# Kernel tuning notes

Hardware: AMD Instinct MI355X
Metric: run time of the kernel (lower is better)

The kernel has to match this reference:

```python
import jax, jax.numpy as jnp
import numpy as np

NEG_INF = -1e9  # matches masked_fill value in torch code
LRELU_ALPHA = 0.2


def setup_inputs() -> dict:
    key = jax.random.key(0)
    k1, k2, k3, k4 = jax.random.split(key, 4)
    B, N, F_IN, H, DK = 4, 2048, 128, 4, 32
    x = jax.random.normal(k1, (B, N, F_IN), dtype=jnp.float32)
    adj = jax.random.randint(k2, (B, N, N), 0, 2, dtype=jnp.int32)
    # xavier-ish scaled params
    W = jax.random.normal(k3, (H, F_IN, DK), dtype=jnp.float32) * (1.0 / np.sqrt(F_IN))
    a = jax.random.normal(k4, (H, 2 * DK, 1), dtype=jnp.float32) * (1.0 / np.sqrt(2 * DK))
    return {"x": x, "adj": adj, "W": W, "a": a}


def reference(x, adj, W, a):
    B, N, _ = x.shape
    H, _, DK = W.shape
    # h: (B, H, N, DK)
    h = jnp.einsum('bni,hio->bhno', x, W)
    # Split attention vector: e[b,h,i,j] = h_i.a_l + h_j.a_r  (avoids O(N^2 * 2d) concat)
    a_l = a[:, :DK, 0]   # (H, DK)
    a_r = a[:, DK:, 0]   # (H, DK)
    el = jnp.einsum('bhnd,hd->bhn', h, a_l)  # (B, H, N)
    er = jnp.einsum('bhnd,hd->bhn', h, a_r)  # (B, H, N)
    e = el[:, :, :, None] + er[:, :, None, :]          # (B, H, N, N)
    e = jax.nn.leaky_relu(e, negative_slope=LRELU_ALPHA)
    e = jnp.where(adj[:, None, :, :] == 0, NEG_INF, e)
    alpha = jax.nn.softmax(e, axis=-1)                 # dropout is identity (eval)
    h_prime = jnp.einsum('bhij,bhjd->bhid', alpha, h)  # (B, H, N, DK)
    # torch code does h_prime.view(B, N, -1) on contiguous (B,H,N,DK): raw reshape
    out = h_prime.reshape(B, N, H * DK)
    return out
```

## Files before the change

kernel.cpp:

```cpp
#include <hip/hip_runtime.h>
#include <stdint.h>

#define LOG2E 1.4426950408889634f

typedef __bf16 v8bf __attribute__((ext_vector_type(8)));
typedef float v16f __attribute__((ext_vector_type(16)));

static constexpr int B = 4, N = 2048, FIN = 128, H = 4, DK = 32;
static constexpr int IT = N / 32;

__device__ __forceinline__ float exp2_fast(float x) {
#if __has_builtin(__builtin_amdgcn_exp2f)
  return __builtin_amdgcn_exp2f(x);
#else
  float r;
  asm("v_exp_f32 %0, %1" : "=v"(r) : "v"(x));
  return r;
#endif
}

__device__ __forceinline__ unsigned int bf16_rne(float f) {
  unsigned int u = __builtin_bit_cast(unsigned int, f);
  u += 0x7FFFu + ((u >> 16) & 1u);
  return u >> 16;
}

__global__ __launch_bounds__(256) void k_prep(const float* __restrict__ x,
                                              const float* __restrict__ W,
                                              unsigned short* __restrict__ xb,
                                              unsigned short* __restrict__ wtb) {
  int idx = blockIdx.x * 256 + threadIdx.x;
  constexpr int TX = B * N * FIN;
  if (idx < TX) {
    xb[idx] = (unsigned short)bf16_rne(x[idx]);
  } else {
    int j = idx - TX;
    int h = j >> 12, r = j & 4095, d = r >> 7, f = r & 127;
    wtb[j] = (unsigned short)bf16_rne(W[(h * FIN + f) * DK + d]);
  }
}

__global__ __launch_bounds__(256) void k_hproj(const unsigned short* __restrict__ xb,
                                               const unsigned short* __restrict__ wtb,
                                               const float* __restrict__ a,
                                               unsigned short* __restrict__ h_t,
                                               float* __restrict__ el,
                                               float* __restrict__ er) {
  int blk = blockIdx.x;
  int b = blk >> 6, it = blk & 63;
  int tid = threadIdx.x;
  int head = tid >> 6, lane = tid & 63;
  int lrow = lane & 31, kh = lane >> 5;
  int bh = b * H + head;
  int n = it * 32 + lrow;
  const unsigned short* xp = xb + (b * N + n) * FIN + kh * 8;
  const unsigned short* wp = wtb + (head * DK + lrow) * FIN + kh * 8;
  v16f acc = {};
#pragma unroll
  for (int s = 0; s < FIN / 16; ++s) {
    v8bf av = __builtin_bit_cast(v8bf, *(const int4*)(wp + s * 16));
    v8bf bv = __builtin_bit_cast(v8bf, *(const int4*)(xp + s * 16));
    acc = __builtin_amdgcn_mfma_f32_32x32x16_bf16(av, bv, acc, 0, 0, 0);
  }
  float pel = 0.f, per = 0.f;
#pragma unroll
  for (int r = 0; r < 16; ++r) {
    int d = (r & 3) + 8 * (r >> 2) + 4 * kh;
    float hv = acc[r];
    h_t[(bh * DK + d) * N + n] = (unsigned short)bf16_rne(hv);
    pel = fmaf(hv, a[head * 2 * DK + d], pel);
    per = fmaf(hv, a[head * 2 * DK + DK + d], per);
  }
  pel += __shfl_xor(pel, 32);
  per += __shfl_xor(per, 32);
  if (kh == 0) {
    el[bh * N + n] = pel * LOG2E;
    er[bh * N + n] = per * LOG2E;
  }
}

__global__ __launch_bounds__(1024, 8) void k_attn(const int* __restrict__ adj,
                                                  const unsigned short* __restrict__ h_t,
                                                  const float* __restrict__ el,
                                                  const float* __restrict__ er,
                                                  float* __restrict__ pnum,
                                                  float* __restrict__ pden) {
  __shared__ float part4[4][H][1024];
  __shared__ float lsh4[4][H][32];
  int blk = blockIdx.x;
  int bit = blk >> 1, jh = blk & 1;
  int b = bit >> 6, it = bit & 63;
  int tid = threadIdx.x;
  int wave = tid >> 6;
  int head = wave & 3, jq = wave >> 2;
  int lane = tid & 63, lrow = lane & 31, kh = lane >> 5;
  int ig = it * 32 + lrow, bh = b * H + head;

  float eli = el[bh * N + ig];
  int j0 = jh * 1024 + jq * 256 + kh * 8;
  const float* erp = er + bh * N + j0;
  const unsigned short* hp = h_t + (size_t)(bh * DK + lrow) * N + j0;
  const int* ap = adj + ((size_t)(b * N + ig)) * N + j0;

  v16f acc = {};
  float lsum = 0.f;
  int4 A0 = *(const int4*)ap;
  int4 A1 = *(const int4*)(ap + 4);
#pragma unroll
  for (int s = 0; s < 16; ++s) {
    int o = s * 16;
    int4 a0 = A0, a1 = A1;
    if (s + 1 < 16) {
      A0 = *(const int4*)(ap + o + 16);
      A1 = *(const int4*)(ap + o + 20);
    }
    float4 ea = *(const float4*)(erp + o);
    float4 eb = *(const float4*)(erp + o + 4);
    int4 hb = *(const int4*)(hp + o);
    float ev[8] = {ea.x, ea.y, ea.z, ea.w, eb.x, eb.y, eb.z, eb.w};
    int aw[8] = {a0.x, a0.y, a0.z, a0.w, a1.x, a1.y, a1.z, a1.w};
    unsigned ub[8];
#pragma unroll
    for (int k = 0; k < 8; ++k) {
      float tt = eli + ev[k];
      tt = fmaxf(tt, 0.2f * tt);
      float pv = exp2_fast(tt);
      unsigned u = __builtin_bit_cast(unsigned, pv) & 0xFFFF0000u;
      u = aw[k] ? u : 0u;
      ub[k] = u;
      lsum += __builtin_bit_cast(float, u);
    }
    unsigned u0 = __builtin_amdgcn_perm(ub[1], ub[0], 0x07060302u);
    unsigned u1 = __builtin_amdgcn_perm(ub[3], ub[2], 0x07060302u);
    unsigned u2 = __builtin_amdgcn_perm(ub[5], ub[4], 0x07060302u);
    unsigned u3 = __builtin_amdgcn_perm(ub[7], ub[6], 0x07060302u);
    uint4 au = {u0, u1, u2, u3};
    v8bf av = __builtin_bit_cast(v8bf, au);
    v8bf hv = __builtin_bit_cast(v8bf, hb);
    acc = __builtin_amdgcn_mfma_f32_32x32x16_bf16(av, hv, acc, 0, 0, 0);
  }

  lsum += __shfl_xor(lsum, 32);
  if (lane < 32) lsh4[jq][head][lane] = lsum;
#pragma unroll
  for (int r = 0; r < 16; ++r) {
    int rowl = (r & 3) + 8 * (r >> 2) + 4 * kh;
    part4[jq][head][rowl * 32 + lrow] = acc[r];
  }
  __syncthreads();

  int e = tid * 4;
  int rh = e >> 10, rr = e & 1023;
  float4 q0 = *(const float4*)&part4[0][rh][rr];
  float4 q1 = *(const float4*)&part4[1][rh][rr];
  float4 q2 = *(const float4*)&part4[2][rh][rr];
  float4 q3 = *(const float4*)&part4[3][rh][rr];
  float4 s4;
  s4.x = (q0.x + q1.x) + (q2.x + q3.x);
  s4.y = (q0.y + q1.y) + (q2.y + q3.y);
  s4.z = (q0.z + q1.z) + (q2.z + q3.z);
  s4.w = (q0.w + q1.w) + (q2.w + q3.w);
  *(float4*)&pnum[(size_t)blk * 4096 + e] = s4;
  if (tid < 128) {
    float d = (lsh4[0][tid >> 5][tid & 31] + lsh4[1][tid >> 5][tid & 31]) +
              (lsh4[2][tid >> 5][tid & 31] + lsh4[3][tid >> 5][tid & 31]);
    pden[blk * 128 + tid] = d;
  }
}

__global__ __launch_bounds__(1024) void k_final(const float* __restrict__ pnum,
                                                const float* __restrict__ pden,
                                                float* __restrict__ out) {
  int bit = blockIdx.x;
  int b = bit >> 6, it = bit & 63;
  int tid = threadIdx.x;
  int e = tid * 4;
  int rh = e >> 10, ri = (e >> 5) & 31, rd = e & 31;
  size_t p0 = (size_t)(bit * 2) * 4096 + e;
  float4 n0 = *(const float4*)&pnum[p0];
  float4 n1 = *(const float4*)&pnum[p0 + 4096];
  float d = pden[bit * 2 * 128 + rh * 32 + ri] + pden[(bit * 2 + 1) * 128 + rh * 32 + ri];
  float inv = 1.0f / d;
  float4 o;
  o.x = (n0.x + n1.x) * inv;
  o.y = (n0.y + n1.y) * inv;
  o.z = (n0.z + n1.z) * inv;
  o.w = (n0.w + n1.w) * inv;
  *(float4*)&out[(size_t)((b * H + rh) * N + it * 32 + ri) * DK + rd] = o;
}

extern "C" void kernel_launch(void* const* d_in, const int* in_sizes, int n_in,
                              void* d_out, int out_size, void* d_ws, size_t ws_size,
                              hipStream_t stream) {
  const float* x = (const float*)d_in[0];
  const int* adj = (const int*)d_in[1];
  const float* W = (const float*)d_in[2];
  const float* a = (const float*)d_in[3];
  float* out = (float*)d_out;
  char* ws = (char*)d_ws;

  unsigned short* h_t = (unsigned short*)(ws);
  float* el = (float*)(ws + 0x200000);
  float* er = (float*)(ws + 0x220000);
  unsigned short* wtb = (unsigned short*)(ws + 0x240000);
  unsigned short* xb = (unsigned short*)(ws + 0x250000);
  float* pnum = (float*)(ws + 0x450000);
  float* pden = (float*)(ws + 0xC50000);

  hipLaunchKernelGGL(k_prep, dim3((B * N * FIN + H * DK * FIN) / 256), dim3(256), 0, stream,
                     x, W, xb, wtb);
  hipLaunchKernelGGL(k_hproj, dim3(B * IT), dim3(256), 0, stream, xb, wtb, a, h_t, el, er);
  hipLaunchKernelGGL(k_attn, dim3(B * IT * 2), dim3(1024), 0, stream, adj, h_t, el, er, pnum, pden);
  hipLaunchKernelGGL(k_final, dim3(B * IT), dim3(1024), 0, stream, pnum, pden, out);
}
```

Before: 158.2 us.

## Pack adjacency into bitmask in prep kernel and read bits in attention

The prep kernel now also compresses the int32 adjacency matrix into a 1-bit-per-entry mask using wave ballots. The attention kernel reads 8 mask words per lane instead of streaming the full int32 rows, and tests bits to zero masked probabilities. Previously each of the four head waves re-read the same adjacency rows, so the goal is to cut that redundant global traffic. The adjacency prefetch in the loop is replaced by prefetching er and h_t. It adds one full pass over adjacency in the prep kernel plus a small workspace buffer.

Result: faster. 135.9 us (-14.1%).

```diff
diff --git a/kernel.cpp b/kernel.cpp
--- a/kernel.cpp
+++ b/kernel.cpp
@@ -8,6 +8,8 @@
 
 static constexpr int B = 4, N = 2048, FIN = 128, H = 4, DK = 32;
 static constexpr int IT = N / 32;
+static constexpr int PACK_BLOCKS = B * N * N / 1024;
+static constexpr int PREP_BLOCKS = (B * N * FIN + H * DK * FIN) / 256;
 
 __device__ __forceinline__ float exp2_fast(float x) {
 #if __has_builtin(__builtin_amdgcn_exp2f)
@@ -25,11 +27,32 @@
   return u >> 16;
 }
 
-__global__ __launch_bounds__(256) void k_prep(const float* __restrict__ x,
+__global__ __launch_bounds__(256) void k_prep(const int* __restrict__ adj,
+                                              const float* __restrict__ x,
                                               const float* __restrict__ W,
+                                              unsigned int* __restrict__ adjb,
                                               unsigned short* __restrict__ xb,
                                               unsigned short* __restrict__ wtb) {
-  int idx = blockIdx.x * 256 + threadIdx.x;
+  int bid = blockIdx.x;
+  int tid = threadIdx.x;
+  if (bid < PACK_BLOCKS) {
+    int wid = (bid * 256 + tid) >> 6;
+    int lane = tid & 63;
+    const int* p = adj + (size_t)wid * 256 + lane;
+    unsigned long long m0 = __ballot(p[0] != 0);
+    unsigned long long m1 = __ballot(p[64] != 0);
+    unsigned long long m2 = __ballot(p[128] != 0);
+    unsigned long long m3 = __ballot(p[192] != 0);
+    if (lane == 0) {
+      uint4 v0 = {(unsigned)m0, (unsigned)(m0 >> 32), (unsigned)m1, (unsigned)(m1 >> 32)};
+      uint4 v1 = {(unsigned)m2, (unsigned)(m2 >> 32), (unsigned)m3, (unsigned)(m3 >> 32)};
+      uint4* dst = (uint4*)(adjb + (size_t)wid * 8);
+      dst[0] = v0;
+      dst[1] = v1;
+    }
+    return;
+  }
+  int idx = (bid - PACK_BLOCKS) * 256 + tid;
   constexpr int TX = B * N * FIN;
   if (idx < TX) {
     xb[idx] = (unsigned short)bf16_rne(x[idx]);
@@ -79,7 +102,7 @@
   }
 }
 
-__global__ __launch_bounds__(1024, 8) void k_attn(const int* __restrict__ adj,
+__global__ __launch_bounds__(1024, 8) void k_attn(const unsigned int* __restrict__ adjb,
                                                   const unsigned short* __restrict__ h_t,
                                                   const float* __restrict__ el,
                                                   const float* __restrict__ er,
@@ -100,25 +123,29 @@
   int j0 = jh * 1024 + jq * 256 + kh * 8;
   const float* erp = er + bh * N + j0;
   const unsigned short* hp = h_t + (size_t)(bh * DK + lrow) * N + j0;
-  const int* ap = adj + ((size_t)(b * N + ig)) * N + j0;
+
+  const uint4* abp = (const uint4*)(adjb + (size_t)(b * N + ig) * 64 + jh * 32 + jq * 8);
+  uint4 ab0 = abp[0], ab1 = abp[1];
+  unsigned adw[8] = {ab0.x, ab0.y, ab0.z, ab0.w, ab1.x, ab1.y, ab1.z, ab1.w};
+  int shkh = kh * 8;
 
   v16f acc = {};
   float lsum = 0.f;
-  int4 A0 = *(const int4*)ap;
-  int4 A1 = *(const int4*)(ap + 4);
+  float4 Ea = *(const float4*)erp;
+  float4 Eb = *(const float4*)(erp + 4);
+  int4 Hb = *(const int4*)hp;
 #pragma unroll
   for (int s = 0; s < 16; ++s) {
-    int o = s * 16;
-    int4 a0 = A0, a1 = A1;
+    float4 ea = Ea, eb = Eb;
+    int4 hb = Hb;
     if (s + 1 < 16) {
-      A0 = *(const int4*)(ap + o + 16);
-      A1 = *(const int4*)(ap + o + 20);
+      int o = (s + 1) * 16;
+      Ea = *(const float4*)(erp + o);
+      Eb = *(const float4*)(erp + o + 4);
+      Hb = *(const int4*)(hp + o);
     }
-    float4 ea = *(const float4*)(erp + o);
-    float4 eb = *(const float4*)(erp + o + 4);
-    int4 hb = *(const int4*)(hp + o);
+    unsigned mb = (adw[s >> 1] >> (((s & 1) * 16) + shkh)) & 0xFFu;
     float ev[8] = {ea.x, ea.y, ea.z, ea.w, eb.x, eb.y, eb.z, eb.w};
-    int aw[8] = {a0.x, a0.y, a0.z, a0.w, a1.x, a1.y, a1.z, a1.w};
     unsigned ub[8];
 #pragma unroll
     for (int k = 0; k < 8; ++k) {
@@ -126,7 +153,7 @@
       tt = fmaxf(tt, 0.2f * tt);
       float pv = exp2_fast(tt);
       unsigned u = __builtin_bit_cast(unsigned, pv) & 0xFFFF0000u;
-      u = aw[k] ? u : 0u;
+      u = (mb & (1u << k)) ? u : 0u;
       ub[k] = u;
       lsum += __builtin_bit_cast(float, u);
     }
@@ -203,13 +230,14 @@
   float* el = (float*)(ws + 0x200000);
   float* er = (float*)(ws + 0x220000);
   unsigned short* wtb = (unsigned short*)(ws + 0x240000);
-  unsigned short* xb = (unsigned short*)(ws + 0x250000);
-  float* pnum = (float*)(ws + 0x450000);
-  float* pden = (float*)(ws + 0xC50000);
-
-  hipLaunchKernelGGL(k_prep, dim3((B * N * FIN + H * DK * FIN) / 256), dim3(256), 0, stream,
-                     x, W, xb, wtb);
+  unsigned int* adjb = (unsigned int*)(ws + 0x250000);
+  unsigned short* xb = (unsigned short*)(ws + 0x450000);
+  float* pnum = (float*)(ws + 0x650000);
+  float* pden = (float*)(ws + 0xE50000);
+
+  hipLaunchKernelGGL(k_prep, dim3(PACK_BLOCKS + PREP_BLOCKS), dim3(256), 0, stream,
+                     adj, x, W, adjb, xb, wtb);
   hipLaunchKernelGGL(k_hproj, dim3(B * IT), dim3(256), 0, stream, xb, wtb, a, h_t, el, er);
-  hipLaunchKernelGGL(k_attn, dim3(B * IT * 2), dim3(1024), 0, stream, adj, h_t, el, er, pnum, pden);
+  hipLaunchKernelGGL(k_attn, dim3(B * IT * 2), dim3(1024), 0, stream, adjb, h_t, el, er, pnum, pden);
   hipLaunchKernelGGL(k_final, dim3(B * IT), dim3(1024), 0, stream, pnum, pden, out);
 }
```
